# Kernel optimization log

Measured on AMD Instinct MI355X. Metric: run time of the kernel, lower is better.

The kernel has to match this reference:

```python
import jax, jax.numpy as jnp
import numpy as np

BS, N, D, H = 4, 2048, 512, 8
DK = D // H
XAVIER_STD = float(np.sqrt(2.0 / (D + D)))  # xavier_normal_, gain=1


def setup_inputs() -> dict:
    key = jax.random.key(0)
    ks = jax.random.split(key, 10)
    Q = jax.random.normal(ks[0], (BS, N, D), jnp.float32)
    K = jax.random.normal(ks[1], (BS, N, D), jnp.float32)
    V = jax.random.normal(ks[2], (BS, N, D), jnp.float32)
    q_mas = jax.random.randint(ks[3], (BS, N, 1), 0, 2).astype(jnp.float32)
    k_mas = jax.random.randint(ks[4], (BS, N, 1), 0, 2).astype(jnp.float32)
    # 0/1 attention mask; force self-edges so no row is fully masked (avoids NaN softmax)
    att_mas = jax.random.randint(ks[5], (BS, N, N), 0, 2).astype(jnp.float32)
    att_mas = jnp.maximum(att_mas, jnp.eye(N, dtype=jnp.float32)[None])
    WQ = jax.random.normal(ks[6], (D, D), jnp.float32) * XAVIER_STD
    WK = jax.random.normal(ks[7], (D, D), jnp.float32) * XAVIER_STD
    WV = jax.random.normal(ks[8], (D, D), jnp.float32) * XAVIER_STD
    WO = jax.random.normal(ks[9], (D, D), jnp.float32) * XAVIER_STD
    return {"Q": Q, "K": K, "V": V, "q_mas": q_mas, "k_mas": k_mas,
            "att_mas": att_mas, "WQ": WQ, "WK": WK, "WV": WV, "WO": WO}


def reference(Q, K, V, q_mas, k_mas, att_mas, WQ, WK, WV, WO):
    bs, n, d = Q.shape
    h, dk = H, DK
    qm = q_mas.reshape(bs, 1, n, 1)  # (bs,1,n,1)
    km = k_mas.reshape(bs, 1, n, 1)
    # nn.Linear (no bias): x @ W.T ; split heads -> (bs,h,n,dk); apply pre-masks
    Qh = qm * (Q @ WQ.T).reshape(bs, n, h, dk).transpose(0, 2, 1, 3)
    Kh = km * (K @ WK.T).reshape(bs, n, h, dk).transpose(0, 2, 1, 3)
    Vh = km * (V @ WV.T).reshape(bs, n, h, dk).transpose(0, 2, 1, 3)
    scores = jnp.einsum('bhqd,bhkd->bhqk', Qh, Kh) / jnp.sqrt(jnp.float32(dk))
    mas = att_mas.reshape(bs, 1, n, n)
    scores = jnp.where(mas.astype(bool), scores, -jnp.inf)
    attn = jax.nn.softmax(scores, axis=-1) * mas
    y = jnp.einsum('bhqk,bhkd->bhqd', attn, Vh) * km  # post-mask (note: km over query dim, as in source)
    y = y.transpose(0, 2, 1, 3).reshape(bs, n, d)
    y = (y @ WO.T) * k_mas.reshape(bs, n, 1)
    return y
```

## Files before the change

### kernel.cpp

```cpp
#include <hip/hip_runtime.h>


#define BS_    4
#define NSEQ   2048
#define DMODEL 512
#define NH     8
#define DKH    64
#define MROWS  (BS_ * NSEQ)

typedef unsigned short ushort_t;
typedef __attribute__((ext_vector_type(8))) short short8;
typedef __attribute__((ext_vector_type(4))) float floatx4;

__device__ __forceinline__ ushort_t f2bf(float f) {
    unsigned int x = __builtin_bit_cast(unsigned int, f);
    unsigned int lsb = (x >> 16) & 1u;
    x += 0x7fffu + lsb;
    return (ushort_t)(x >> 16);
}
__device__ __forceinline__ floatx4 mfma_bf16(short8 a, short8 b, floatx4 c) {
    return __builtin_amdgcn_mfma_f32_16x16x32_bf16(a, b, c, 0, 0, 0);
}
__device__ __forceinline__ void gld16(const ushort_t* g, ushort_t* l) {
    __builtin_amdgcn_global_load_lds(
        (const __attribute__((address_space(1))) unsigned int*)g,
        (__attribute__((address_space(3))) unsigned int*)l, 16, 0, 0);
}

__global__ __launch_bounds__(256) void cvt3_kernel(const float* __restrict__ a,
                                                   const float* __restrict__ b,
                                                   const float* __restrict__ c,
                                                   ushort_t* __restrict__ dst, int n4) {
    const float* src = (blockIdx.y == 0) ? a : (blockIdx.y == 1) ? b : c;
    ushort_t* d = dst + (size_t)blockIdx.y * ((size_t)n4 * 4);
    const int i = blockIdx.x * blockDim.x + threadIdx.x;
    const float4 v = ((const float4*)src)[i];
    ushort4 o;
    o.x = f2bf(v.x); o.y = f2bf(v.y); o.z = f2bf(v.z); o.w = f2bf(v.w);
    ((ushort4*)d)[i] = o;
}

__global__ __launch_bounds__(256) void cvt4_kernel(const float* __restrict__ a,
                                                   const float* __restrict__ b,
                                                   const float* __restrict__ c,
                                                   const float* __restrict__ e,
                                                   ushort_t* __restrict__ dst, int n4) {
    const float* src = (blockIdx.y == 0) ? a : (blockIdx.y == 1) ? b
                     : (blockIdx.y == 2) ? c : e;
    ushort_t* d = dst + (size_t)blockIdx.y * ((size_t)n4 * 4);
    const int i = blockIdx.x * blockDim.x + threadIdx.x;
    const float4 v = ((const float4*)src)[i];
    ushort4 o;
    o.x = f2bf(v.x); o.y = f2bf(v.y); o.z = f2bf(v.z); o.w = f2bf(v.w);
    ((ushort4*)d)[i] = o;
}

__global__ __launch_bounds__(256) void gemm_proj(const ushort_t* __restrict__ Xall,
                                                 const ushort_t* __restrict__ Wall,
                                                 const float* __restrict__ qmas,
                                                 const float* __restrict__ kmas,
                                                 ushort_t* __restrict__ Qh,
                                                 ushort_t* __restrict__ Kh,
                                                 ushort_t* __restrict__ Vt) {
    __shared__ ushort_t As[128 * 32];
    __shared__ ushort_t Bs[128 * 32];
    const int z = blockIdx.z;
    const ushort_t* X  = Xall + (size_t)z * MROWS * DMODEL;
    const ushort_t* Wb = Wall + (size_t)z * DMODEL * DMODEL;
    const float* rowmask = (z == 0) ? qmas : kmas;

    const int tid  = threadIdx.x;
    const int wave = tid >> 6;
    const int lane = tid & 63;
    const int l16  = lane & 15;
    const int quad = lane >> 4;
    const int wr   = wave >> 1;
    const int wc   = wave & 1;
    const int m0   = blockIdx.x * 128;
    const int n0   = blockIdx.y * 128;
    const int crow = lane >> 2;
    const int koff = (lane & 3) * 8;

    floatx4 acc[4][4];
#pragma unroll
    for (int t = 0; t < 4; ++t)
#pragma unroll
        for (int u = 0; u < 4; ++u) acc[t][u] = (floatx4){0.f, 0.f, 0.f, 0.f};

    for (int k0 = 0; k0 < DMODEL; k0 += 32) {
#pragma unroll
        for (int c2 = 0; c2 < 2; ++c2) {
            const int c = wave * 2 + c2;
            gld16(X  + (size_t)(m0 + c * 16 + crow) * DMODEL + k0 + koff, &As[c * 512]);
            gld16(Wb + (size_t)(n0 + c * 16 + crow) * DMODEL + k0 + koff, &Bs[c * 512]);
        }
        __syncthreads();
        short8 a[4], b[4];
#pragma unroll
        for (int t = 0; t < 4; ++t)
            a[t] = *(const short8*)&As[(wr * 64 + t * 16 + l16) * 32 + quad * 8];
#pragma unroll
        for (int u = 0; u < 4; ++u)
            b[u] = *(const short8*)&Bs[(wc * 64 + u * 16 + l16) * 32 + quad * 8];
#pragma unroll
        for (int t = 0; t < 4; ++t)
#pragma unroll
            for (int u = 0; u < 4; ++u) acc[t][u] = mfma_bf16(a[t], b[u], acc[t][u]);
        __syncthreads();
    }

    float rm[4][4];
#pragma unroll
    for (int t = 0; t < 4; ++t)
#pragma unroll
        for (int r = 0; r < 4; ++r)
            rm[t][r] = rowmask[m0 + wr * 64 + t * 16 + quad * 4 + r];

    const int bb    = m0 >> 11;
    const int nbase = (m0 & (NSEQ - 1)) + wr * 64;
#pragma unroll
    for (int t = 0; t < 4; ++t) {
#pragma unroll
        for (int u = 0; u < 4; ++u) {
            const int d = n0 + wc * 64 + u * 16 + l16;
            const int h = d >> 6, cc = d & 63;
            if (z < 2) {
                ushort_t* dst = (z == 0) ? Qh : Kh;
#pragma unroll
                for (int r = 0; r < 4; ++r) {
                    const int n = nbase + t * 16 + quad * 4 + r;
                    dst[((size_t)(bb * NH + h) * NSEQ + n) * DKH + cc] =
                        f2bf(acc[t][u][r] * rm[t][r]);
                }
            } else {
                ushort4 pk;
                pk.x = f2bf(acc[t][u][0] * rm[t][0]);
                pk.y = f2bf(acc[t][u][1] * rm[t][1]);
                pk.z = f2bf(acc[t][u][2] * rm[t][2]);
                pk.w = f2bf(acc[t][u][3] * rm[t][3]);
                const int n = nbase + t * 16 + quad * 4;
                *(ushort4*)(Vt + ((size_t)(bb * NH + h) * DKH + cc) * NSEQ + n) = pk;
            }
        }
    }
}

__global__ __launch_bounds__(256) void gemm_out(const ushort_t* __restrict__ X,
                                                const ushort_t* __restrict__ Wb,
                                                const float* __restrict__ rowmask,
                                                float* __restrict__ dst) {
    __shared__ ushort_t As[128 * 32];
    __shared__ ushort_t Bs[128 * 32];
    const int tid  = threadIdx.x;
    const int wave = tid >> 6;
    const int lane = tid & 63;
    const int l16  = lane & 15;
    const int quad = lane >> 4;
    const int wr   = wave >> 1;
    const int wc   = wave & 1;
    const int m0   = blockIdx.x * 128;
    const int n0   = blockIdx.y * 128;
    const int crow = lane >> 2;
    const int koff = (lane & 3) * 8;

    floatx4 acc[4][4];
#pragma unroll
    for (int t = 0; t < 4; ++t)
#pragma unroll
        for (int u = 0; u < 4; ++u) acc[t][u] = (floatx4){0.f, 0.f, 0.f, 0.f};

    for (int k0 = 0; k0 < DMODEL; k0 += 32) {
#pragma unroll
        for (int c2 = 0; c2 < 2; ++c2) {
            const int c = wave * 2 + c2;
            gld16(X  + (size_t)(m0 + c * 16 + crow) * DMODEL + k0 + koff, &As[c * 512]);
            gld16(Wb + (size_t)(n0 + c * 16 + crow) * DMODEL + k0 + koff, &Bs[c * 512]);
        }
        __syncthreads();
        short8 a[4], b[4];
#pragma unroll
        for (int t = 0; t < 4; ++t)
            a[t] = *(const short8*)&As[(wr * 64 + t * 16 + l16) * 32 + quad * 8];
#pragma unroll
        for (int u = 0; u < 4; ++u)
            b[u] = *(const short8*)&Bs[(wc * 64 + u * 16 + l16) * 32 + quad * 8];
#pragma unroll
        for (int t = 0; t < 4; ++t)
#pragma unroll
            for (int u = 0; u < 4; ++u) acc[t][u] = mfma_bf16(a[t], b[u], acc[t][u]);
        __syncthreads();
    }

#pragma unroll
    for (int t = 0; t < 4; ++t) {
#pragma unroll
        for (int r = 0; r < 4; ++r) {
            const int m = m0 + wr * 64 + t * 16 + quad * 4 + r;
            const float rm = rowmask[m];
#pragma unroll
            for (int u = 0; u < 4; ++u) {
                const int d = n0 + wc * 64 + u * 16 + l16;
                dst[(size_t)m * DMODEL + d] = acc[t][u][r] * rm;
            }
        }
    }
}

__global__ __launch_bounds__(256) void attn_kernel(const ushort_t* __restrict__ Qh,
                                                   const ushort_t* __restrict__ Kh,
                                                   const ushort_t* __restrict__ Vt,
                                                   const float* __restrict__ amas,
                                                   const float* __restrict__ kmas,
                                                   ushort_t* __restrict__ y) {
    __shared__ __align__(16) ushort_t Ks[128 * 72];
    __shared__ __align__(16) ushort_t Vs[64 * 136];
    __shared__ __align__(16) ushort_t Ps[4][16 * 136];

    const int tid  = threadIdx.x;
    const int wave = tid >> 6;
    const int lane = tid & 63;
    const int l16  = lane & 15;
    const int quad = lane >> 4;
    const int h    = blockIdx.y;
    const int b    = blockIdx.z;
    const int qw   = blockIdx.x * 64 + wave * 16;

    const ushort_t* Kb = Kh + (size_t)(b * NH + h) * NSEQ * DKH;
    const ushort_t* Vb = Vt + (size_t)(b * NH + h) * DKH * NSEQ;
    const float*    Am = amas + (size_t)(b * NSEQ + qw) * NSEQ;

    const ushort_t* Qp = Qh + ((size_t)((b * NH + h) * NSEQ) + qw + l16) * DKH + quad * 8;
    const short8 qfa = *(const short8*)Qp;
    const short8 qfb = *(const short8*)(Qp + 32);

    float lpart[4] = {0.f, 0.f, 0.f, 0.f};
    floatx4 accO[4];
#pragma unroll
    for (int ct = 0; ct < 4; ++ct) accO[ct] = (floatx4){0.f, 0.f, 0.f, 0.f};

    const float CEXP = 0.18033688011112042f;

    for (int kt = 0; kt < NSEQ / 128; ++kt) {
        const int k0 = kt * 128;

        short8 kv[4], vv[4];
#pragma unroll
        for (int i = 0; i < 4; ++i) {
            const int c = tid + i * 256;
            kv[i] = *(const short8*)(Kb + (size_t)(k0 + (c >> 3)) * DKH + (c & 7) * 8);
        }
#pragma unroll
        for (int i = 0; i < 4; ++i) {
            const int c = tid + i * 256;
            vv[i] = *(const short8*)(Vb + (size_t)(c >> 4) * NSEQ + k0 + (c & 15) * 8);
        }
        float av[8][4];
#pragma unroll
        for (int fr = 0; fr < 8; ++fr)
#pragma unroll
            for (int r = 0; r < 4; ++r)
                av[fr][r] = Am[(size_t)(quad * 4 + r) * NSEQ + k0 + fr * 16 + l16];

        __syncthreads();
#pragma unroll
        for (int i = 0; i < 4; ++i) {
            const int c = tid + i * 256;
            *(short8*)&Ks[(c >> 3) * 72 + (c & 7) * 8] = kv[i];
        }
#pragma unroll
        for (int i = 0; i < 4; ++i) {
            const int c = tid + i * 256;
            *(short8*)&Vs[(c >> 4) * 136 + (c & 15) * 8] = vv[i];
        }
        __syncthreads();

        floatx4 S[8];
#pragma unroll
        for (int fr = 0; fr < 8; ++fr) {
            const short8 ka = *(const short8*)&Ks[(fr * 16 + l16) * 72 + quad * 8];
            const short8 kb = *(const short8*)&Ks[(fr * 16 + l16) * 72 + 32 + quad * 8];
            floatx4 s = {0.f, 0.f, 0.f, 0.f};
            s = mfma_bf16(qfa, ka, s);
            s = mfma_bf16(qfb, kb, s);
            S[fr] = s;
        }

#pragma unroll
        for (int fr = 0; fr < 8; ++fr) {
#pragma unroll
            for (int r = 0; r < 4; ++r) {
                const float p = av[fr][r] * exp2f(S[fr][r] * CEXP);
                lpart[r] += p;
                Ps[wave][(quad * 4 + r) * 136 + fr * 16 + l16] = f2bf(p);
            }
        }

        __builtin_amdgcn_wave_barrier();
        short8 pf[4];
#pragma unroll
        for (int kf = 0; kf < 4; ++kf)
            pf[kf] = *(const short8*)&Ps[wave][l16 * 136 + kf * 32 + quad * 8];
        __builtin_amdgcn_wave_barrier();

#pragma unroll
        for (int ct = 0; ct < 4; ++ct) {
#pragma unroll
            for (int kf = 0; kf < 4; ++kf) {
                const short8 vb = *(const short8*)&Vs[(ct * 16 + l16) * 136 + kf * 32 + quad * 8];
                accO[ct] = mfma_bf16(pf[kf], vb, accO[ct]);
            }
        }
    }

#pragma unroll
    for (int r = 0; r < 4; ++r) {
        float l = lpart[r];
        l += __shfl_xor(l, 1);
        l += __shfl_xor(l, 2);
        l += __shfl_xor(l, 4);
        l += __shfl_xor(l, 8);
        const int q = qw + quad * 4 + r;
        const float scale = kmas[b * NSEQ + q] / l;
#pragma unroll
        for (int ct = 0; ct < 4; ++ct) {
            y[(size_t)(b * NSEQ + q) * DMODEL + h * DKH + ct * 16 + l16] =
                f2bf(accO[ct][r] * scale);
        }
    }
}

extern "C" void kernel_launch(void* const* d_in, const int* in_sizes, int n_in,
                              void* d_out, int out_size, void* d_ws, size_t ws_size,
                              hipStream_t stream) {
    (void)in_sizes; (void)n_in; (void)out_size; (void)ws_size;
    const float* Q  = (const float*)d_in[0];
    const float* K  = (const float*)d_in[1];
    const float* V  = (const float*)d_in[2];
    const float* qm = (const float*)d_in[3];
    const float* km = (const float*)d_in[4];
    const float* am = (const float*)d_in[5];
    const float* WQ = (const float*)d_in[6];
    const float* WK = (const float*)d_in[7];
    const float* WV = (const float*)d_in[8];
    const float* WO = (const float*)d_in[9];

    const size_t XN = (size_t)MROWS * DMODEL;
    const size_t WN = (size_t)DMODEL * DMODEL;
    ushort_t* Xbf = (ushort_t*)d_ws;
    ushort_t* Wbf = Xbf + 3 * XN;
    ushort_t* WOb = Wbf + 3 * WN;
    ushort_t* Qh  = Wbf + 4 * WN;
    ushort_t* Kh  = Qh + XN;
    ushort_t* Vt  = Kh + XN;
    ushort_t* y   = Vt + XN;
    float* out = (float*)d_out;

    hipLaunchKernelGGL(cvt3_kernel, dim3(4096, 3), dim3(256), 0, stream,
                       Q, K, V, Xbf, (int)(XN / 4));
    hipLaunchKernelGGL(cvt4_kernel, dim3(256, 4), dim3(256), 0, stream,
                       WQ, WK, WV, WO, Wbf, (int)(WN / 4));

    hipLaunchKernelGGL(gemm_proj, dim3(MROWS / 128, DMODEL / 128, 3), dim3(256), 0, stream,
                       Xbf, Wbf, qm, km, Qh, Kh, Vt);

    hipLaunchKernelGGL(attn_kernel, dim3(NSEQ / 64, NH, BS_), dim3(256), 0, stream,
                       Qh, Kh, Vt, am, km, y);

    hipLaunchKernelGGL(gemm_out, dim3(MROWS / 128, DMODEL / 128), dim3(256), 0, stream,
                       y, WOb, km, out);
}
```

Before: 287.9 us.

## Pack attention mask to bits once and use transposed score layout

A new kernel packs the float32 attention mask into 32-bit words once, before attention. Each attention block then reads a few bytes per row tile instead of the full float mask, which was previously re-read by all 8 heads. The exp scaling constant is folded into the Q projection. The score MFMA operands are swapped so each lane holds contiguous keys for one query, which lets P be written with packed bf16 conversion and bitmask selection. This adds an extra kernel pass over the 64MB mask and reuses the Xbf workspace, which is safe only because the projections have already finished by then.

New measurement: 292.8 us. No clear change (+1.7%).

```diff
diff --git a/kernel.cpp b/kernel.cpp
--- a/kernel.cpp
+++ b/kernel.cpp
@@ -7,6 +7,7 @@
 #define NH     8
 #define DKH    64
 #define MROWS  (BS_ * NSEQ)
+#define NW32   (NSEQ / 32)
 
 typedef unsigned short ushort_t;
 typedef __attribute__((ext_vector_type(8))) short short8;
@@ -25,6 +26,11 @@
     __builtin_amdgcn_global_load_lds(
         (const __attribute__((address_space(1))) unsigned int*)g,
         (__attribute__((address_space(3))) unsigned int*)l, 16, 0, 0);
+}
+__device__ __forceinline__ unsigned int cvt_pk_bf16(float lo, float hi) {
+    unsigned int r;
+    asm("v_cvt_pk_bf16_f32 %0, %1, %2" : "=v"(r) : "v"(lo), "v"(hi));
+    return r;
 }
 
 __global__ __launch_bounds__(256) void cvt3_kernel(const float* __restrict__ a,
@@ -55,6 +61,22 @@
     ((ushort4*)d)[i] = o;
 }
 
+__global__ __launch_bounds__(256) void mask_pack(const float* __restrict__ am,
+                                                 unsigned int* __restrict__ mb) {
+    const int t = blockIdx.x * 256 + threadIdx.x;
+    const float4* src = (const float4*)am + (size_t)t * 8;
+    unsigned int m = 0;
+#pragma unroll
+    for (int j = 0; j < 8; ++j) {
+        const float4 v = src[j];
+        m |= (v.x != 0.f ? 1u : 0u) << (4 * j);
+        m |= (v.y != 0.f ? 1u : 0u) << (4 * j + 1);
+        m |= (v.z != 0.f ? 1u : 0u) << (4 * j + 2);
+        m |= (v.w != 0.f ? 1u : 0u) << (4 * j + 3);
+    }
+    mb[t] = m;
+}
+
 __global__ __launch_bounds__(256) void gemm_proj(const ushort_t* __restrict__ Xall,
                                                  const ushort_t* __restrict__ Wall,
                                                  const float* __restrict__ qmas,
@@ -115,6 +137,12 @@
 #pragma unroll
         for (int r = 0; r < 4; ++r)
             rm[t][r] = rowmask[m0 + wr * 64 + t * 16 + quad * 4 + r];
+    if (z == 0) {
+#pragma unroll
+        for (int t = 0; t < 4; ++t)
+#pragma unroll
+            for (int r = 0; r < 4; ++r) rm[t][r] *= 0.18033688011112042f;
+    }
 
     const int bb    = m0 >> 11;
     const int nbase = (m0 & (NSEQ - 1)) + wr * 64;
@@ -209,7 +237,7 @@
 __global__ __launch_bounds__(256) void attn_kernel(const ushort_t* __restrict__ Qh,
                                                    const ushort_t* __restrict__ Kh,
                                                    const ushort_t* __restrict__ Vt,
-                                                   const float* __restrict__ amas,
+                                                   const unsigned int* __restrict__ Mb,
                                                    const float* __restrict__ kmas,
                                                    ushort_t* __restrict__ y) {
     __shared__ __align__(16) ushort_t Ks[128 * 72];
@@ -227,18 +255,16 @@
 
     const ushort_t* Kb = Kh + (size_t)(b * NH + h) * NSEQ * DKH;
     const ushort_t* Vb = Vt + (size_t)(b * NH + h) * DKH * NSEQ;
-    const float*    Am = amas + (size_t)(b * NSEQ + qw) * NSEQ;
+    const unsigned int* Mrow = Mb + ((size_t)(b * NSEQ + qw) + l16) * NW32;
 
     const ushort_t* Qp = Qh + ((size_t)((b * NH + h) * NSEQ) + qw + l16) * DKH + quad * 8;
     const short8 qfa = *(const short8*)Qp;
     const short8 qfb = *(const short8*)(Qp + 32);
 
-    float lpart[4] = {0.f, 0.f, 0.f, 0.f};
+    float lpart = 0.f;
     floatx4 accO[4];
 #pragma unroll
     for (int ct = 0; ct < 4; ++ct) accO[ct] = (floatx4){0.f, 0.f, 0.f, 0.f};
-
-    const float CEXP = 0.18033688011112042f;
 
     for (int kt = 0; kt < NSEQ / 128; ++kt) {
         const int k0 = kt * 128;
@@ -254,12 +280,7 @@
             const int c = tid + i * 256;
             vv[i] = *(const short8*)(Vb + (size_t)(c >> 4) * NSEQ + k0 + (c & 15) * 8);
         }
-        float av[8][4];
-#pragma unroll
-        for (int fr = 0; fr < 8; ++fr)
-#pragma unroll
-            for (int r = 0; r < 4; ++r)
-                av[fr][r] = Am[(size_t)(quad * 4 + r) * NSEQ + k0 + fr * 16 + l16];
+        const uint4 mw = *(const uint4*)(Mrow + (k0 >> 5));
 
         __syncthreads();
 #pragma unroll
@@ -280,19 +301,30 @@
             const short8 ka = *(const short8*)&Ks[(fr * 16 + l16) * 72 + quad * 8];
             const short8 kb = *(const short8*)&Ks[(fr * 16 + l16) * 72 + 32 + quad * 8];
             floatx4 s = {0.f, 0.f, 0.f, 0.f};
-            s = mfma_bf16(qfa, ka, s);
-            s = mfma_bf16(qfb, kb, s);
+            s = mfma_bf16(ka, qfa, s);
+            s = mfma_bf16(kb, qfb, s);
             S[fr] = s;
         }
 
+        const unsigned int wsh[4] = {mw.x >> (quad * 4), mw.y >> (quad * 4),
+                                     mw.z >> (quad * 4), mw.w >> (quad * 4)};
 #pragma unroll
         for (int fr = 0; fr < 8; ++fr) {
+            float p[4];
 #pragma unroll
             for (int r = 0; r < 4; ++r) {
-                const float p = av[fr][r] * exp2f(S[fr][r] * CEXP);
-                lpart[r] += p;
-                Ps[wave][(quad * 4 + r) * 136 + fr * 16 + l16] = f2bf(p);
+                const int bitp = ((fr & 1) << 4) + r;
+                const unsigned int mm =
+                    (unsigned int)((int)(wsh[fr >> 1] << (31 - bitp)) >> 31);
+                const float e = exp2f(S[fr][r]);
+                const unsigned int pb = __builtin_bit_cast(unsigned int, e) & mm;
+                p[r] = __builtin_bit_cast(float, pb);
+                lpart += p[r];
             }
+            uint2 pk;
+            pk.x = cvt_pk_bf16(p[0], p[1]);
+            pk.y = cvt_pk_bf16(p[2], p[3]);
+            *(uint2*)&Ps[wave][l16 * 136 + fr * 16 + quad * 4] = pk;
         }
 
         __builtin_amdgcn_wave_barrier();
@@ -312,14 +344,13 @@
         }
     }
 
+    float lfull = lpart;
+    lfull += __shfl_xor(lfull, 16);
+    lfull += __shfl_xor(lfull, 32);
 #pragma unroll
     for (int r = 0; r < 4; ++r) {
-        float l = lpart[r];
-        l += __shfl_xor(l, 1);
-        l += __shfl_xor(l, 2);
-        l += __shfl_xor(l, 4);
-        l += __shfl_xor(l, 8);
         const int q = qw + quad * 4 + r;
+        const float l = __shfl(lfull, quad * 4 + r);
         const float scale = kmas[b * NSEQ + q] / l;
 #pragma unroll
         for (int ct = 0; ct < 4; ++ct) {
@@ -353,6 +384,7 @@
     ushort_t* Kh  = Qh + XN;
     ushort_t* Vt  = Kh + XN;
     ushort_t* y   = Vt + XN;
+    unsigned int* Mbits = (unsigned int*)Xbf;
     float* out = (float*)d_out;
 
     hipLaunchKernelGGL(cvt3_kernel, dim3(4096, 3), dim3(256), 0, stream,
@@ -363,8 +395,11 @@
     hipLaunchKernelGGL(gemm_proj, dim3(MROWS / 128, DMODEL / 128, 3), dim3(256), 0, stream,
                        Xbf, Wbf, qm, km, Qh, Kh, Vt);
 
+    hipLaunchKernelGGL(mask_pack, dim3((BS_ * NSEQ * NSEQ / 32) / 256), dim3(256), 0, stream,
+                       am, Mbits);
+
     hipLaunchKernelGGL(attn_kernel, dim3(NSEQ / 64, NH, BS_), dim3(256), 0, stream,
-                       Qh, Kh, Vt, am, km, y);
+                       Qh, Kh, Vt, Mbits, km, y);
 
     hipLaunchKernelGGL(gemm_out, dim3(MROWS / 128, DMODEL / 128), dim3(256), 0, stream,
                        y, WOb, km, out);
```
